# Kernel optimization log

Measured on AMD Instinct MI355X. Metric: run time of the kernel, lower is better.

The kernel has to match this reference:

```python
import jax, jax.numpy as jnp
import numpy as np
from jax import lax

TOP_K = 4
N_GROUP = 4
TOPK_GROUP = 2
ROUTED_SCALE = 2.5
NEG_INF = -1e9


def setup_inputs() -> dict:
    key = jax.random.key(0)
    ks = jax.random.split(key, 6)
    B, S, H, I, E = 2, 2048, 1024, 512, 16
    x = jax.random.normal(ks[0], (B, S, H), dtype=jnp.float32)
    router_weight = jax.random.normal(ks[1], (E, H), dtype=jnp.float32) * 0.02
    router_bias = jnp.zeros((E,), dtype=jnp.float32)
    w_gate = jax.random.normal(ks[2], (E, I, H), dtype=jnp.float32) * 0.02
    w_up = jax.random.normal(ks[3], (E, I, H), dtype=jnp.float32) * 0.02
    w_down = jax.random.normal(ks[4], (E, H, I), dtype=jnp.float32) * 0.02
    return {"x": x, "router_weight": router_weight, "router_bias": router_bias,
            "w_gate": w_gate, "w_up": w_up, "w_down": w_down}


def _route(xf, router_weight, router_bias):
    # DeepSeek-V3 sigmoid router with group-limited top-k.
    T = xf.shape[0]
    E = router_weight.shape[0]
    logits = xf @ router_weight.T                      # [T, E]
    scores = jax.nn.sigmoid(logits)                    # [T, E]
    s_choice = scores + router_bias                    # bias used only for selection
    per_group = E // N_GROUP
    sg = s_choice.reshape(T, N_GROUP, per_group)
    group_scores = lax.top_k(sg, 2)[0].sum(-1)         # [T, n_group] sum of top-2
    _, gidx = lax.top_k(group_scores, TOPK_GROUP)      # [T, topk_group]
    gmask = jnp.zeros((T, N_GROUP), dtype=bool).at[jnp.arange(T)[:, None], gidx].set(True)
    masked = jnp.where(gmask[:, :, None], sg, NEG_INF).reshape(T, E)
    _, topk_idx = lax.top_k(masked, TOP_K)             # [T, top_k]
    w = jnp.take_along_axis(scores, topk_idx, axis=1)  # original sigmoid scores
    w = w / (w.sum(-1, keepdims=True) + 1e-20) * ROUTED_SCALE
    combine = jnp.zeros((T, E), dtype=xf.dtype).at[jnp.arange(T)[:, None], topk_idx].add(w)
    return combine


def reference(x, router_weight, router_bias, w_gate, w_up, w_down):
    B, S, H = x.shape
    E = w_gate.shape[0]
    xf = x.reshape(-1, H)                              # [T, H]
    combine = _route(xf, router_weight, router_bias)   # [T, E]
    # Grouped-GEMM SwiGLU experts expressed as per-expert dense GEMMs with
    # combine-weighted accumulation (same math as sort+grouped-mm+scatter).
    out = jnp.zeros_like(xf)
    for e in range(E):
        g = xf @ w_gate[e].T                           # [T, I]
        u = xf @ w_up[e].T                             # [T, I]
        y_e = (jax.nn.silu(g) * u) @ w_down[e].T       # [T, H]
        out = out + combine[:, e:e + 1] * y_e
    return out.reshape(B, S, H)
```

## Files before the change

kernel.cpp:

```cpp
#include <hip/hip_runtime.h>
#include <stdint.h>

#define T_TOK   4096
#define H_DIM   1024
#define I_DIM   512
#define E_EXP   16
#define TOPK    4
#define NTILEMAX 144

typedef __attribute__((ext_vector_type(8))) short bf16x8;
typedef __attribute__((ext_vector_type(4))) float f32x4;
typedef __attribute__((ext_vector_type(8))) unsigned short ushort8;

__device__ __forceinline__ unsigned short f2bf(float f) {
  unsigned u = __float_as_uint(f);
  u = u + 0x7fffu + ((u >> 16) & 1u);
  return (unsigned short)(u >> 16);
}
__device__ __forceinline__ float bf2f(unsigned short s) {
  return __uint_as_float(((unsigned)s) << 16);
}

__device__ __forceinline__ void gload_lds16(const void* g, void* l) {
  __builtin_amdgcn_global_load_lds(
      (const __attribute__((address_space(1))) unsigned int*)g,
      (__attribute__((address_space(3))) unsigned int*)l, 16, 0, 0);
}

__device__ __forceinline__ void cvt_seg8(const float* __restrict__ src,
                                         unsigned short* __restrict__ dst,
                                         int n8, int tid0, int stride) {
  for (int i = tid0; i < n8; i += stride) {
    float4 v0 = ((const float4*)src)[2 * i];
    float4 v1 = ((const float4*)src)[2 * i + 1];
    ushort8 o;
    o[0] = f2bf(v0.x); o[1] = f2bf(v0.y); o[2] = f2bf(v0.z); o[3] = f2bf(v0.w);
    o[4] = f2bf(v1.x); o[5] = f2bf(v1.y); o[6] = f2bf(v1.z); o[7] = f2bf(v1.w);
    ((ushort8*)dst)[i] = o;
  }
}

__global__ __launch_bounds__(256) void cvt_w_kernel(
    const float* __restrict__ wg, unsigned short* __restrict__ wgb,
    const float* __restrict__ wu, unsigned short* __restrict__ wub,
    const float* __restrict__ wd, unsigned short* __restrict__ wdb) {
  const int tid0 = blockIdx.x * blockDim.x + threadIdx.x;
  const int stride = gridDim.x * blockDim.x;
  cvt_seg8(wg, wgb, E_EXP * I_DIM * H_DIM / 8, tid0, stride);
  cvt_seg8(wu, wub, E_EXP * I_DIM * H_DIM / 8, tid0, stride);
  cvt_seg8(wd, wdb, E_EXP * H_DIM * I_DIM / 8, tid0, stride);
}

__global__ __launch_bounds__(256) void logits_sel_kernel(
    const float* __restrict__ x, const float* __restrict__ rw,
    const float* __restrict__ rb, unsigned short* __restrict__ xb,
    int* __restrict__ tidx, float* __restrict__ tw) {
  const int t = blockIdx.x * 4 + (threadIdx.x >> 6);
  const int lane = threadIdx.x & 63;
  const float* xr = x + (size_t)t * H_DIM;

  float4 xv[4];
#pragma unroll
  for (int i = 0; i < 4; ++i) xv[i] = ((const float4*)xr)[i * 64 + lane];

  unsigned short* xrow = xb + (size_t)t * H_DIM;
#pragma unroll
  for (int i = 0; i < 4; ++i) {
    ushort4 o;
    o.x = f2bf(xv[i].x); o.y = f2bf(xv[i].y);
    o.z = f2bf(xv[i].z); o.w = f2bf(xv[i].w);
    ((ushort4*)xrow)[i * 64 + lane] = o;
  }

  float myl[E_EXP];
#pragma unroll
  for (int g = 0; g < 4; ++g) {
    float acc[4] = {0.f, 0.f, 0.f, 0.f};
#pragma unroll
    for (int e4 = 0; e4 < 4; ++e4) {
      const float* wrow = rw + (size_t)(g * 4 + e4) * H_DIM;
#pragma unroll
      for (int i = 0; i < 4; ++i) {
        float4 wv = ((const float4*)wrow)[i * 64 + lane];
        acc[e4] = fmaf(xv[i].x, wv.x, acc[e4]);
        acc[e4] = fmaf(xv[i].y, wv.y, acc[e4]);
        acc[e4] = fmaf(xv[i].z, wv.z, acc[e4]);
        acc[e4] = fmaf(xv[i].w, wv.w, acc[e4]);
      }
    }
#pragma unroll
    for (int e4 = 0; e4 < 4; ++e4) {
#pragma unroll
      for (int off = 32; off > 0; off >>= 1) acc[e4] += __shfl_down(acc[e4], off, 64);
      myl[g * 4 + e4] = acc[e4];
    }
  }
  if (lane != 0) return;

  float sc[E_EXP], sch[E_EXP];
#pragma unroll
  for (int e = 0; e < E_EXP; ++e) {
    sc[e] = 1.f / (1.f + expf(-myl[e]));
    sch[e] = sc[e] + rb[e];
  }

  float gsum[4];
#pragma unroll
  for (int g = 0; g < 4; ++g) {
    float m1 = -3e38f, m2 = -3e38f;
#pragma unroll
    for (int j = 0; j < 4; ++j) {
      float v = sch[g * 4 + j];
      if (v > m1) { m2 = m1; m1 = v; } else if (v > m2) { m2 = v; }
    }
    gsum[g] = m1 + m2;
  }
  int g1 = 0;
  for (int g = 1; g < 4; ++g) if (gsum[g] > gsum[g1]) g1 = g;
  int g2 = -1;
  for (int g = 0; g < 4; ++g)
    if (g != g1 && (g2 < 0 || gsum[g] > gsum[g2])) g2 = g;

  float cand[E_EXP];
#pragma unroll
  for (int e = 0; e < E_EXP; ++e)
    cand[e] = ((e >> 2) == g1 || (e >> 2) == g2) ? sch[e] : -1e9f;

  int idx[TOPK]; float wv[TOPK]; float wsum = 0.f;
#pragma unroll
  for (int k = 0; k < TOPK; ++k) {
    int bi = 0; float bv = cand[0];
#pragma unroll
    for (int e = 1; e < E_EXP; ++e) if (cand[e] > bv) { bv = cand[e]; bi = e; }
    idx[k] = bi; cand[bi] = -3e38f;
    wv[k] = sc[bi];
    wsum += wv[k];
  }
  float scale = 2.5f / (wsum + 1e-20f);
#pragma unroll
  for (int k = 0; k < TOPK; ++k) {
    tidx[t * 4 + k] = idx[k];
    tw[t * 4 + k] = wv[k] * scale;
  }
}

__global__ __launch_bounds__(256) void plan_kernel(
    const int* __restrict__ tidx, int* __restrict__ offg,
    int* __restrict__ toffg, int* __restrict__ rowmap,
    int* __restrict__ rowtok) {
  const int e = blockIdx.x, tid = threadIdx.x;
  const int lane = tid & 63, wv = tid >> 6;
  __shared__ int histo[E_EXP];
  __shared__ int wsum[4];
  __shared__ int srun;
  if (tid < E_EXP) histo[tid] = 0;
  if (tid == 0) srun = 0;
  __syncthreads();
  for (int i = tid; i < T_TOK * TOPK; i += 256)
    atomicAdd(&histo[tidx[i]], 1);
  __syncthreads();

  if (e == 0 && tid == 0) {
    int a = 0, tt = 0;
    for (int q = 0; q < E_EXP; ++q) {
      offg[q] = a; toffg[q] = tt;
      a += histo[q];
      tt += (histo[q] + 127) >> 7;
    }
    offg[E_EXP] = a; toffg[E_EXP] = tt;
  }
  int base = 0;
  for (int q = 0; q < e; ++q) base += histo[q];

  for (int c = 0; c < T_TOK * TOPK / 256; ++c) {
    const int i = c * 256 + tid;
    const bool f = (tidx[i] == e);
    unsigned long long m = __ballot(f);
    int wpre = __popcll(m & ((1ull << lane) - 1ull));
    if (lane == 63) wsum[wv] = wpre + (f ? 1 : 0);
    __syncthreads();
    const int run = srun;
    int pre = 0, tot = 0;
#pragma unroll
    for (int w = 0; w < 4; ++w) {
      int v = wsum[w];
      if (w < wv) pre += v;
      tot += v;
    }
    if (f) {
      const int pos = base + run + pre + wpre;
      rowmap[i] = pos;
      rowtok[pos] = i >> 2;
    }
    __syncthreads();
    if (tid == 0) srun = run + tot;
  }
}

__device__ __forceinline__ int find_expert(const int* __restrict__ toff, int tile) {
  int e = 0;
#pragma unroll
  for (int q = 1; q <= E_EXP; ++q) e += (toff[q] <= tile);
  return e;
}

__global__ __launch_bounds__(256, 3) void gateup_kernel(
    const unsigned short* __restrict__ xbf,
    const unsigned short* __restrict__ wgbf,
    const unsigned short* __restrict__ wubf,
    const int* __restrict__ rowtok, const int* __restrict__ off,
    const int* __restrict__ toff,
    unsigned short* __restrict__ hbuf) {
  const int bid = (int)blockIdx.x;
  const int work = (bid & 7) * NTILEMAX + (bid >> 3);
  const int tile = work >> 3, tn = work & 7;
  if (tile >= toff[E_EXP]) return;
  const int e = find_expert(toff, tile);
  const int tm = tile - toff[e];
  const int seg0 = off[e];
  const int nrows = off[e + 1] - seg0;

  __shared__ __align__(16) unsigned short As[128 * 64];
  __shared__ __align__(16) unsigned short Gs[64 * 64];
  __shared__ __align__(16) unsigned short Us[64 * 64];
  __shared__ int ids[128];

  const int tid = threadIdx.x;
  if (tid < 128) {
    int r = tm * 128 + tid;
    ids[tid] = rowtok[seg0 + (r < nrows ? r : 0)];
  }
  __syncthreads();

  const int col8 = tid & 7;
  const int r0 = tid >> 3;
  const int csrc = (col8 ^ (r0 & 7)) * 8;
  int tokA[4];
#pragma unroll
  for (int j = 0; j < 4; ++j) tokA[j] = ids[j * 32 + r0];

  const unsigned short* wg = wgbf + (size_t)e * I_DIM * H_DIM + (size_t)(tn * 64) * H_DIM;
  const unsigned short* wu = wubf + (size_t)e * I_DIM * H_DIM + (size_t)(tn * 64) * H_DIM;

  f32x4 accg[4][2], accu[4][2];
#pragma unroll
  for (int m = 0; m < 4; ++m)
#pragma unroll
    for (int n = 0; n < 2; ++n) { accg[m][n] = (f32x4)0.f; accu[m][n] = (f32x4)0.f; }

  const int lane = tid & 63, wid = tid >> 6;
  const int wr = wid >> 1, wc = wid & 1;
  const int frow = lane & 15, fr7 = frow & 7;
  const int kc = lane >> 4;

  for (int kt = 0; kt < H_DIM / 64; ++kt) {
    const int kb = kt * 64 + csrc;
    __syncthreads();
#pragma unroll
    for (int j = 0; j < 4; ++j)
      gload_lds16(xbf + ((size_t)tokA[j] * H_DIM + kb), (char*)As + (j * 256 + tid) * 16);
#pragma unroll
    for (int j = 0; j < 2; ++j) {
      gload_lds16(wg + ((size_t)(j * 32 + r0) * H_DIM + kb), (char*)Gs + (j * 256 + tid) * 16);
      gload_lds16(wu + ((size_t)(j * 32 + r0) * H_DIM + kb), (char*)Us + (j * 256 + tid) * 16);
    }
    __syncthreads();
#pragma unroll
    for (int kk = 0; kk < 2; ++kk) {
      const int swz = ((kk * 4 + kc) ^ fr7) * 8;
      bf16x8 af[4], bg[2], bu[2];
#pragma unroll
      for (int m = 0; m < 4; ++m)
        af[m] = *(const bf16x8*)&As[(wr * 64 + m * 16 + frow) * 64 + swz];
#pragma unroll
      for (int n = 0; n < 2; ++n) {
        bg[n] = *(const bf16x8*)&Gs[(wc * 32 + n * 16 + frow) * 64 + swz];
        bu[n] = *(const bf16x8*)&Us[(wc * 32 + n * 16 + frow) * 64 + swz];
      }
#pragma unroll
      for (int m = 0; m < 4; ++m)
#pragma unroll
        for (int n = 0; n < 2; ++n) {
          accg[m][n] = __builtin_amdgcn_mfma_f32_16x16x32_bf16(af[m], bg[n], accg[m][n], 0, 0, 0);
          accu[m][n] = __builtin_amdgcn_mfma_f32_16x16x32_bf16(af[m], bu[n], accu[m][n], 0, 0, 0);
        }
    }
  }

  const int lr = (lane >> 4) * 4, lc = lane & 15;
#pragma unroll
  for (int m = 0; m < 4; ++m) {
#pragma unroll
    for (int j = 0; j < 4; ++j) {
      int r = tm * 128 + wr * 64 + m * 16 + lr + j;
      if (r < nrows) {
        size_t rowoff = (size_t)(seg0 + r) * I_DIM;
#pragma unroll
        for (int n = 0; n < 2; ++n) {
          float g = accg[m][n][j];
          float u = accu[m][n][j];
          float hv = g / (1.f + __expf(-g)) * u;
          hbuf[rowoff + tn * 64 + wc * 32 + n * 16 + lc] = f2bf(hv);
        }
      }
    }
  }
}

__global__ __launch_bounds__(256, 3) void down_kernel(
    const unsigned short* __restrict__ hbuf,
    const unsigned short* __restrict__ wdbf,
    const int* __restrict__ off, const int* __restrict__ toff,
    unsigned short* __restrict__ ybuf) {
  const int bid = (int)blockIdx.x;
  const int work = (bid & 7) * NTILEMAX + (bid >> 3);
  const int tile = work >> 3, tn = work & 7;
  if (tile >= toff[E_EXP]) return;
  const int e = find_expert(toff, tile);
  const int tm = tile - toff[e];
  const int seg0 = off[e];
  const int nrows = off[e + 1] - seg0;

  __shared__ __align__(16) unsigned short As[128 * 64];
  __shared__ __align__(16) unsigned short Bs[128 * 64];

  const int tid = threadIdx.x;
  const int col8 = tid & 7;
  const int r0 = tid >> 3;
  const int csrc = (col8 ^ (r0 & 7)) * 8;
  int rowA[4];
#pragma unroll
  for (int j = 0; j < 4; ++j) {
    int r = tm * 128 + j * 32 + r0;
    rowA[j] = seg0 + (r < nrows ? r : nrows - 1);
  }
  const unsigned short* wd = wdbf + (size_t)e * H_DIM * I_DIM + (size_t)(tn * 128) * I_DIM;

  f32x4 acc[4][4];
#pragma unroll
  for (int m = 0; m < 4; ++m)
#pragma unroll
    for (int n = 0; n < 4; ++n) acc[m][n] = (f32x4)0.f;

  const int lane = tid & 63, wid = tid >> 6;
  const int wr = wid >> 1, wc = wid & 1;
  const int frow = lane & 15, fr7 = frow & 7;
  const int kc = lane >> 4;

  for (int kt = 0; kt < I_DIM / 64; ++kt) {
    const int kb = kt * 64 + csrc;
    __syncthreads();
#pragma unroll
    for (int j = 0; j < 4; ++j) {
      gload_lds16(hbuf + ((size_t)rowA[j] * I_DIM + kb), (char*)As + (j * 256 + tid) * 16);
      gload_lds16(wd + ((size_t)(j * 32 + r0) * I_DIM + kb), (char*)Bs + (j * 256 + tid) * 16);
    }
    __syncthreads();
#pragma unroll
    for (int kk = 0; kk < 2; ++kk) {
      const int swz = ((kk * 4 + kc) ^ fr7) * 8;
      bf16x8 af[4], bw[4];
#pragma unroll
      for (int m = 0; m < 4; ++m)
        af[m] = *(const bf16x8*)&As[(wr * 64 + m * 16 + frow) * 64 + swz];
#pragma unroll
      for (int n = 0; n < 4; ++n)
        bw[n] = *(const bf16x8*)&Bs[(wc * 64 + n * 16 + frow) * 64 + swz];
#pragma unroll
      for (int m = 0; m < 4; ++m)
#pragma unroll
        for (int n = 0; n < 4; ++n)
          acc[m][n] = __builtin_amdgcn_mfma_f32_16x16x32_bf16(af[m], bw[n], acc[m][n], 0, 0, 0);
    }
  }

  const int lr = (lane >> 4) * 4, lc = lane & 15;
#pragma unroll
  for (int m = 0; m < 4; ++m) {
#pragma unroll
    for (int j = 0; j < 4; ++j) {
      int r = tm * 128 + wr * 64 + m * 16 + lr + j;
      if (r < nrows) {
        size_t rowoff = (size_t)(seg0 + r) * H_DIM;
#pragma unroll
        for (int n = 0; n < 4; ++n)
          ybuf[rowoff + tn * 128 + wc * 64 + n * 16 + lc] = f2bf(acc[m][n][j]);
      }
    }
  }
}

__global__ __launch_bounds__(256) void combine_kernel(
    const unsigned short* __restrict__ ybuf, const int* __restrict__ rowmap,
    const float* __restrict__ tw, float* __restrict__ out) {
  int t = blockIdx.x, tid = threadIdx.x;
  __shared__ int rloc[4];
  __shared__ float wloc[4];
  if (tid < 4) { rloc[tid] = rowmap[t * 4 + tid]; wloc[tid] = tw[t * 4 + tid]; }
  __syncthreads();
  int c = tid * 4;
  float4 a = {0.f, 0.f, 0.f, 0.f};
#pragma unroll
  for (int k = 0; k < 4; ++k) {
    ushort4 v = *(const ushort4*)&ybuf[(size_t)rloc[k] * H_DIM + c];
    float w = wloc[k];
    a.x += w * bf2f(v.x); a.y += w * bf2f(v.y);
    a.z += w * bf2f(v.z); a.w += w * bf2f(v.w);
  }
  *(float4*)&out[(size_t)t * H_DIM + c] = a;
}

extern "C" void kernel_launch(void* const* d_in, const int* in_sizes, int n_in,
                              void* d_out, int out_size, void* d_ws, size_t ws_size,
                              hipStream_t stream) {
  (void)in_sizes; (void)n_in; (void)out_size; (void)ws_size;
  const float* x  = (const float*)d_in[0];
  const float* rw = (const float*)d_in[1];
  const float* rb = (const float*)d_in[2];
  const float* wg = (const float*)d_in[3];
  const float* wu = (const float*)d_in[4];
  const float* wd = (const float*)d_in[5];
  float* out = (float*)d_out;

  char* base = (char*)d_ws;
  size_t o = 0;
  auto alloc = [&](size_t b) -> void* {
    void* p = base + o;
    o += (b + 255) & ~(size_t)255;
    return p;
  };
  unsigned short* xbf   = (unsigned short*)alloc((size_t)T_TOK * H_DIM * 2);
  unsigned short* wgbf  = (unsigned short*)alloc((size_t)E_EXP * I_DIM * H_DIM * 2);
  unsigned short* wubf  = (unsigned short*)alloc((size_t)E_EXP * I_DIM * H_DIM * 2);
  unsigned short* wdbf  = (unsigned short*)alloc((size_t)E_EXP * H_DIM * I_DIM * 2);
  unsigned short* hbuf  = (unsigned short*)alloc((size_t)T_TOK * TOPK * I_DIM * 2);
  unsigned short* ybuf  = (unsigned short*)alloc((size_t)T_TOK * TOPK * H_DIM * 2);
  int*   tidx   = (int*)alloc((size_t)T_TOK * TOPK * 4);
  float* tw     = (float*)alloc((size_t)T_TOK * TOPK * 4);
  int*   rowmap = (int*)alloc((size_t)T_TOK * TOPK * 4);
  int*   rowtok = (int*)alloc((size_t)T_TOK * TOPK * 4);
  int*   offb   = (int*)alloc(256);
  int*   toffb  = (int*)alloc(256);

  cvt_w_kernel<<<2048, 256, 0, stream>>>(wg, wgbf, wu, wubf, wd, wdbf);

  logits_sel_kernel<<<T_TOK / 4, 256, 0, stream>>>(x, rw, rb, xbf, tidx, tw);
  plan_kernel<<<E_EXP, 256, 0, stream>>>(tidx, offb, toffb, rowmap, rowtok);

  gateup_kernel<<<8 * NTILEMAX, 256, 0, stream>>>(xbf, wgbf, wubf, rowtok, offb, toffb, hbuf);
  down_kernel<<<8 * NTILEMAX, 256, 0, stream>>>(hbuf, wdbf, offb, toffb, ybuf);
  combine_kernel<<<T_TOK, 256, 0, stream>>>(ybuf, rowmap, tw, out);
}
```

Baseline: 163.8 us.

## Fuse gate/up weight bf16 conversion into gateup GEMM with register prefetch

Removes the separate fp32-to-bf16 pass over the gate and up weights. The gateup kernel now loads fp32 weights straight into registers, converts them with packed cvt instructions and stores them to swizzled LDS, and prefetches the next k-tile's weights while the MFMAs run. This drops a 64 MB write and reread of the converted weights. In exchange each gateup block re-reads and re-converts fp32 weights (twice the bytes per tile, many times across M tiles) and uses more registers. Launch bounds are also raised to 4 waves per SIMD for both GEMMs.

```diff
diff --git a/kernel.cpp b/kernel.cpp
--- a/kernel.cpp
+++ b/kernel.cpp
@@ -21,34 +21,31 @@
   return __uint_as_float(((unsigned)s) << 16);
 }
 
+__device__ __forceinline__ unsigned cvtpk(float lo, float hi) {
+  unsigned r;
+  asm("v_cvt_pk_bf16_f32 %0, %1, %2" : "=v"(r) : "v"(lo), "v"(hi));
+  return r;
+}
+
 __device__ __forceinline__ void gload_lds16(const void* g, void* l) {
   __builtin_amdgcn_global_load_lds(
       (const __attribute__((address_space(1))) unsigned int*)g,
       (__attribute__((address_space(3))) unsigned int*)l, 16, 0, 0);
 }
 
-__device__ __forceinline__ void cvt_seg8(const float* __restrict__ src,
-                                         unsigned short* __restrict__ dst,
-                                         int n8, int tid0, int stride) {
+__global__ __launch_bounds__(256) void cvt_wd_kernel(
+    const float* __restrict__ wd, unsigned short* __restrict__ wdb) {
+  const int tid0 = blockIdx.x * blockDim.x + threadIdx.x;
+  const int stride = gridDim.x * blockDim.x;
+  const int n8 = E_EXP * H_DIM * I_DIM / 8;
   for (int i = tid0; i < n8; i += stride) {
-    float4 v0 = ((const float4*)src)[2 * i];
-    float4 v1 = ((const float4*)src)[2 * i + 1];
+    float4 v0 = ((const float4*)wd)[2 * i];
+    float4 v1 = ((const float4*)wd)[2 * i + 1];
     ushort8 o;
     o[0] = f2bf(v0.x); o[1] = f2bf(v0.y); o[2] = f2bf(v0.z); o[3] = f2bf(v0.w);
     o[4] = f2bf(v1.x); o[5] = f2bf(v1.y); o[6] = f2bf(v1.z); o[7] = f2bf(v1.w);
-    ((ushort8*)dst)[i] = o;
-  }
-}
-
-__global__ __launch_bounds__(256) void cvt_w_kernel(
-    const float* __restrict__ wg, unsigned short* __restrict__ wgb,
-    const float* __restrict__ wu, unsigned short* __restrict__ wub,
-    const float* __restrict__ wd, unsigned short* __restrict__ wdb) {
-  const int tid0 = blockIdx.x * blockDim.x + threadIdx.x;
-  const int stride = gridDim.x * blockDim.x;
-  cvt_seg8(wg, wgb, E_EXP * I_DIM * H_DIM / 8, tid0, stride);
-  cvt_seg8(wu, wub, E_EXP * I_DIM * H_DIM / 8, tid0, stride);
-  cvt_seg8(wd, wdb, E_EXP * H_DIM * I_DIM / 8, tid0, stride);
+    ((ushort8*)wdb)[i] = o;
+  }
 }
 
 __global__ __launch_bounds__(256) void logits_sel_kernel(
@@ -204,10 +201,10 @@
   return e;
 }
 
-__global__ __launch_bounds__(256, 3) void gateup_kernel(
+__global__ __launch_bounds__(256, 4) void gateup_kernel(
     const unsigned short* __restrict__ xbf,
-    const unsigned short* __restrict__ wgbf,
-    const unsigned short* __restrict__ wubf,
+    const float* __restrict__ wgf,
+    const float* __restrict__ wuf,
     const int* __restrict__ rowtok, const int* __restrict__ off,
     const int* __restrict__ toff,
     unsigned short* __restrict__ hbuf) {
@@ -235,12 +232,14 @@
   const int col8 = tid & 7;
   const int r0 = tid >> 3;
   const int csrc = (col8 ^ (r0 & 7)) * 8;
+  const int bcol = col8 * 8;
+  const int bdst = (col8 ^ (r0 & 7)) * 8;
   int tokA[4];
 #pragma unroll
   for (int j = 0; j < 4; ++j) tokA[j] = ids[j * 32 + r0];
 
-  const unsigned short* wg = wgbf + (size_t)e * I_DIM * H_DIM + (size_t)(tn * 64) * H_DIM;
-  const unsigned short* wu = wubf + (size_t)e * I_DIM * H_DIM + (size_t)(tn * 64) * H_DIM;
+  const float* wg = wgf + (size_t)e * I_DIM * H_DIM + (size_t)(tn * 64) * H_DIM;
+  const float* wu = wuf + (size_t)e * I_DIM * H_DIM + (size_t)(tn * 64) * H_DIM;
 
   f32x4 accg[4][2], accu[4][2];
 #pragma unroll
@@ -253,18 +252,39 @@
   const int frow = lane & 15, fr7 = frow & 7;
   const int kc = lane >> 4;
 
-  for (int kt = 0; kt < H_DIM / 64; ++kt) {
-    const int kb = kt * 64 + csrc;
+  const int NT = H_DIM / 64;
+  float4 Bg[2][2], Bu[2][2];
+
+  auto loadB = [&](int kt) {
+#pragma unroll
+    for (int j = 0; j < 2; ++j) {
+      const float* gs = wg + (size_t)(j * 32 + r0) * H_DIM + kt * 64 + bcol;
+      const float* us = wu + (size_t)(j * 32 + r0) * H_DIM + kt * 64 + bcol;
+      Bg[j][0] = ((const float4*)gs)[0]; Bg[j][1] = ((const float4*)gs)[1];
+      Bu[j][0] = ((const float4*)us)[0]; Bu[j][1] = ((const float4*)us)[1];
+    }
+  };
+
+  loadB(0);
+  for (int kt = 0; kt < NT; ++kt) {
+    const int kbA = kt * 64 + csrc;
+#pragma unroll
+    for (int j = 0; j < 4; ++j)
+      gload_lds16(xbf + ((size_t)tokA[j] * H_DIM + kbA), (char*)As + (j * 256 + tid) * 16);
+#pragma unroll
+    for (int j = 0; j < 2; ++j) {
+      const int row = j * 32 + r0;
+      uint4 gw, uw;
+      gw.x = cvtpk(Bg[j][0].x, Bg[j][0].y); gw.y = cvtpk(Bg[j][0].z, Bg[j][0].w);
+      gw.z = cvtpk(Bg[j][1].x, Bg[j][1].y); gw.w = cvtpk(Bg[j][1].z, Bg[j][1].w);
+      uw.x = cvtpk(Bu[j][0].x, Bu[j][0].y); uw.y = cvtpk(Bu[j][0].z, Bu[j][0].w);
+      uw.z = cvtpk(Bu[j][1].x, Bu[j][1].y); uw.w = cvtpk(Bu[j][1].z, Bu[j][1].w);
+      *(uint4*)&Gs[row * 64 + bdst] = gw;
+      *(uint4*)&Us[row * 64 + bdst] = uw;
+    }
     __syncthreads();
-#pragma unroll
-    for (int j = 0; j < 4; ++j)
-      gload_lds16(xbf + ((size_t)tokA[j] * H_DIM + kb), (char*)As + (j * 256 + tid) * 16);
-#pragma unroll
-    for (int j = 0; j < 2; ++j) {
-      gload_lds16(wg + ((size_t)(j * 32 + r0) * H_DIM + kb), (char*)Gs + (j * 256 + tid) * 16);
-      gload_lds16(wu + ((size_t)(j * 32 + r0) * H_DIM + kb), (char*)Us + (j * 256 + tid) * 16);
-    }
-    __syncthreads();
+    if (kt + 1 < NT) loadB(kt + 1);
+    __builtin_amdgcn_sched_barrier(0);
 #pragma unroll
     for (int kk = 0; kk < 2; ++kk) {
       const int swz = ((kk * 4 + kc) ^ fr7) * 8;
@@ -285,6 +305,9 @@
           accu[m][n] = __builtin_amdgcn_mfma_f32_16x16x32_bf16(af[m], bu[n], accu[m][n], 0, 0, 0);
         }
     }
+    __builtin_amdgcn_sched_barrier(0);
+    __builtin_amdgcn_s_barrier();
+    __builtin_amdgcn_sched_barrier(0);
   }
 
   const int lr = (lane >> 4) * 4, lc = lane & 15;
@@ -307,7 +330,7 @@
   }
 }
 
-__global__ __launch_bounds__(256, 3) void down_kernel(
+__global__ __launch_bounds__(256, 4) void down_kernel(
     const unsigned short* __restrict__ hbuf,
     const unsigned short* __restrict__ wdbf,
     const int* __restrict__ off, const int* __restrict__ toff,
@@ -430,8 +453,6 @@
     return p;
   };
   unsigned short* xbf   = (unsigned short*)alloc((size_t)T_TOK * H_DIM * 2);
-  unsigned short* wgbf  = (unsigned short*)alloc((size_t)E_EXP * I_DIM * H_DIM * 2);
-  unsigned short* wubf  = (unsigned short*)alloc((size_t)E_EXP * I_DIM * H_DIM * 2);
   unsigned short* wdbf  = (unsigned short*)alloc((size_t)E_EXP * H_DIM * I_DIM * 2);
   unsigned short* hbuf  = (unsigned short*)alloc((size_t)T_TOK * TOPK * I_DIM * 2);
   unsigned short* ybuf  = (unsigned short*)alloc((size_t)T_TOK * TOPK * H_DIM * 2);
@@ -442,12 +463,11 @@
   int*   offb   = (int*)alloc(256);
   int*   toffb  = (int*)alloc(256);
 
-  cvt_w_kernel<<<2048, 256, 0, stream>>>(wg, wgbf, wu, wubf, wd, wdbf);
-
+  cvt_wd_kernel<<<2048, 256, 0, stream>>>(wd, wdbf);
   logits_sel_kernel<<<T_TOK / 4, 256, 0, stream>>>(x, rw, rb, xbf, tidx, tw);
   plan_kernel<<<E_EXP, 256, 0, stream>>>(tidx, offb, toffb, rowmap, rowtok);
 
-  gateup_kernel<<<8 * NTILEMAX, 256, 0, stream>>>(xbf, wgbf, wubf, rowtok, offb, toffb, hbuf);
+  gateup_kernel<<<8 * NTILEMAX, 256, 0, stream>>>(xbf, wg, wu, rowtok, offb, toffb, hbuf);
   down_kernel<<<8 * NTILEMAX, 256, 0, stream>>>(hbuf, wdbf, offb, toffb, ybuf);
   combine_kernel<<<T_TOK, 256, 0, stream>>>(ybuf, rowmap, tw, out);
 }
```

Measured after the change: 191.0 us, median of 2. 16.6% more time.
